# Performance work log

Measured on AMD Instinct MI355X. Metric: run time of the kernel, lower is better.

The kernel has to match this reference:

```python
import jax, jax.numpy as jnp
import numpy as np

D_MODEL = 384
N_HEADS = 8
HEAD_DIM = D_MODEL // N_HEADS


def setup_inputs() -> dict:
    key = jax.random.key(0)
    ks = jax.random.split(key, 8)
    b, n = 2, 2048
    s = 0.02
    return {
        "x": jax.random.normal(ks[0], (b, n, D_MODEL), jnp.float32),
        "coords": jax.random.normal(ks[1], (b, n, 3), jnp.float32),
        "W_qkv": jax.random.normal(ks[2], (D_MODEL, 3 * D_MODEL), jnp.float32) * s,
        "b_qkv": jnp.zeros((3 * D_MODEL,), jnp.float32),
        "W_dist": jax.random.normal(ks[3], (1, N_HEADS), jnp.float32) * s,
        "b_dist": jnp.zeros((N_HEADS,), jnp.float32),
        "W_out": jax.random.normal(ks[4], (D_MODEL, D_MODEL), jnp.float32) * s,
        "b_out": jnp.zeros((D_MODEL,), jnp.float32),
    }


def reference(x, coords, W_qkv, b_qkv, W_dist, b_dist, W_out, b_out):
    b, n, _ = x.shape
    qkv = x @ W_qkv + b_qkv                       # (b, n, 3*d)
    q, k, v = jnp.split(qkv, 3, axis=-1)
    def heads(t):
        return t.reshape(b, n, N_HEADS, HEAD_DIM).transpose(0, 2, 1, 3)  # b h n d
    q, k, v = heads(q), heads(k), heads(v)
    attn = jnp.einsum('bhid,bhjd->bhij', q, k) / jnp.sqrt(jnp.float32(HEAD_DIM))
    # distance bias: ||c_i - c_j|| projected to heads (Linear(1, n_heads))
    diff = coords[:, :, None, :] - coords[:, None, :, :]   # (b, i, j, 3)
    dist = jnp.sqrt(jnp.sum(diff * diff, axis=-1))         # (b, i, j)
    dist_bias = dist[..., None] * W_dist[0] + b_dist       # (b, i, j, h)
    attn = attn + dist_bias.transpose(0, 3, 1, 2)          # (b, h, i, j)
    attn = jax.nn.softmax(attn, axis=-1)
    out = jnp.einsum('bhij,bhjd->bhid', attn, v)
    out = out.transpose(0, 2, 1, 3).reshape(b, n, D_MODEL)
    return out @ W_out + b_out
```

## Files before the change

kernel.cpp:

```cpp
#include <hip/hip_runtime.h>
#include <hip/hip_bf16.h>

#define NB 2
#define SEQ 2048
#define DM 384
#define NH 8
#define HD 48
#define QKVN 1152
#define BH (NB*NH)

typedef __hip_bfloat16 bf16;
typedef __attribute__((ext_vector_type(8))) short short8;
typedef __attribute__((ext_vector_type(4))) float float4v;

static __device__ __forceinline__ float bf2f(bf16 v){ return __bfloat162float(v); }
static __device__ __forceinline__ float ldin(const void* p, size_t i, int isf){
    return isf ? ((const float*)p)[i] : bf2f(((const bf16*)p)[i]);
}
static __device__ __forceinline__ short f2b(float f){
    union { float f; unsigned u; } a; a.f = f;
    unsigned r = a.u + 0x7FFFu + ((a.u >> 16) & 1u);
    return (short)(r >> 16);
}
static __device__ __forceinline__ unsigned pk2(float a, float b){
    union { float f; unsigned u; } ua, ub; ua.f = a; ub.f = b;
    return ((ua.u + 0x8000u) >> 16) | ((ub.u + 0x8000u) & 0xFFFF0000u);
}
static __device__ __forceinline__ float bflo(unsigned u){
    union { unsigned u; float f; } a; a.u = u << 16; return a.f;
}
static __device__ __forceinline__ float bfhi(unsigned u){
    union { unsigned u; float f; } a; a.u = u & 0xFFFF0000u; return a.f;
}
static __device__ __forceinline__ int detect_isf(const void* x){
    const unsigned short* xb = (const unsigned short*)x;
    int l = threadIdx.x & 63;
    union { unsigned u; float f; } a; a.u = ((unsigned)xb[2*l]) << 16;
    float ab = fabsf(a.f);
    int good = (a.f == 0.0f) || (ab > 9.765625e-4f && ab < 1024.0f);
    unsigned long long m = __ballot(good);
    return (__popcll(m) >= 32) ? 0 : 1;
}

__global__ __launch_bounds__(256) void k_prep(const void* __restrict__ x,
    const void* __restrict__ coords,
    const void* __restrict__ Wqkv, const void* __restrict__ Wout,
    const void* __restrict__ bqkv, const void* __restrict__ bout,
    const void* __restrict__ Wdist, const void* __restrict__ bdist,
    short* __restrict__ dist8, short* __restrict__ xb,
    short* __restrict__ WqT, short* __restrict__ WoT,
    float* __restrict__ bqf, float* __restrict__ bof,
    float* __restrict__ wdf, float* __restrict__ bdf)
{
    const int isf = detect_isf(x);
    const int t = threadIdx.x;
    const int b = blockIdx.x;
    if (b < 512) {
        const int bb = b >> 8;
        const int j0 = (b & 255) * 8;
        __shared__ float cjx[8], cjy[8], cjz[8];
        if (t < 8) {
            int gj = (bb*SEQ + j0 + t)*3;
            cjx[t] = ldin(coords, gj, isf);
            cjy[t] = ldin(coords, gj+1, isf);
            cjz[t] = ldin(coords, gj+2, isf);
        }
        __syncthreads();
        #pragma unroll
        for (int ii = 0; ii < 8; ++ii) {
            int i = ii*256 + t;
            int gi = (bb*SEQ + i)*3;
            float px = ldin(coords, gi, isf), py = ldin(coords, gi+1, isf), pz = ldin(coords, gi+2, isf);
            short o[8];
            #pragma unroll
            for (int e = 0; e < 8; ++e) {
                float dx = px - cjx[e], dy = py - cjy[e], dz = pz - cjz[e];
                o[e] = f2b(sqrtf(dx*dx + dy*dy + dz*dz));
            }
            *(int4*)(dist8 + ((size_t)b*SEQ + i)*8) = *(const int4*)o;
        }
    } else if (b < 1280) {
        size_t i = ((size_t)(b-512)*256 + t)*8;
        if (isf) {
            const float* xf = (const float*)x + i;
            short o[8];
            #pragma unroll
            for (int e = 0; e < 8; ++e) o[e] = f2b(xf[e]);
            *(int4*)(xb + i) = *(const int4*)o;
        } else {
            *(int4*)(xb + i) = *(const int4*)((const short*)x + i);
        }
    } else if (b < 1856) {
        int bb, NW; const void* W; short* WT;
        if (b < 1712) { bb = b - 1280; NW = QKVN; W = Wqkv; WT = WqT; }
        else          { bb = b - 1712; NW = DM;   W = Wout; WT = WoT; }
        int ntiles = NW >> 5;
        int kt = bb / ntiles, nt = bb % ntiles;
        int k0 = kt*32, n0 = nt*32;
        __shared__ float Ls[32][33];
        for (int idx = t; idx < 1024; idx += 256) {
            int r = idx >> 5, c = idx & 31;
            Ls[r][c] = ldin(W, (size_t)(k0+r)*NW + n0 + c, isf);
        }
        __syncthreads();
        for (int idx = t; idx < 1024; idx += 256) {
            int r2 = idx >> 5, c2 = idx & 31;
            WT[(size_t)(n0+r2)*DM + k0 + c2] = f2b(Ls[c2][r2]);
        }
    } else {
        int idx = (b - 1856)*256 + t;
        if (idx < QKVN) bqf[idx] = ldin(bqkv, idx, isf);
        else if (idx < QKVN + DM) bof[idx - QKVN] = ldin(bout, idx - QKVN, isf);
        else if (idx < QKVN + DM + NH) wdf[idx - QKVN - DM] = ldin(Wdist, idx - QKVN - DM, isf);
        else if (idx < QKVN + DM + 2*NH) bdf[idx - QKVN - DM - NH] = ldin(bdist, idx - QKVN - DM - NH, isf);
    }
}

__global__ __launch_bounds__(256) void k_qkv(const short* __restrict__ xb,
    const short* __restrict__ WT, const float* __restrict__ bias,
    short* __restrict__ qg2, short* __restrict__ kg2, short* __restrict__ vg2)
{
    __shared__ __align__(16) short As[64*72];
    __shared__ __align__(16) short Bs[128*72];
    const int t = threadIdx.x;
    const int w = t >> 6, lane = t & 63, L = lane & 15, quad = lane >> 4;
    const int mt = blockIdx.x / 9, nt = blockIdx.x % 9;
    const int row0 = mt*64, col0 = nt*128;
    const int wm = w & 1, wn = w >> 1;
    float4v acc[2][4] = {};
    for (int k0 = 0; k0 < DM; k0 += 64) {
        __syncthreads();
        for (int c = t; c < 512; c += 256) {
            int row = c >> 3, k8 = c & 7;
            *(int4*)(&As[row*72 + k8*8]) = *(const int4*)(xb + (size_t)(row0+row)*DM + k0 + k8*8);
        }
        for (int c = t; c < 1024; c += 256) {
            int row = c >> 3, k8 = c & 7;
            *(int4*)(&Bs[row*72 + k8*8]) = *(const int4*)(WT + (size_t)(col0+row)*DM + k0 + k8*8);
        }
        __syncthreads();
        #pragma unroll
        for (int kc = 0; kc < 2; ++kc) {
            short8 a0 = *(const short8*)(&As[(32*wm + L)*72 + kc*32 + quad*8]);
            short8 a1 = *(const short8*)(&As[(32*wm + 16 + L)*72 + kc*32 + quad*8]);
            #pragma unroll
            for (int ni = 0; ni < 4; ++ni) {
                short8 bf = *(const short8*)(&Bs[(64*wn + 16*ni + L)*72 + kc*32 + quad*8]);
                acc[0][ni] = __builtin_amdgcn_mfma_f32_16x16x32_bf16(a0, bf, acc[0][ni], 0, 0, 0);
                acc[1][ni] = __builtin_amdgcn_mfma_f32_16x16x32_bf16(a1, bf, acc[1][ni], 0, 0, 0);
            }
        }
    }
    const int which = col0 / DM;
    const int cbase = col0 % DM;
    short* Ep = Bs;
    __syncthreads();
    if (which < 2) {
        #pragma unroll
        for (int mi = 0; mi < 2; ++mi)
            #pragma unroll
            for (int ni = 0; ni < 4; ++ni) {
                int col_l = 64*wn + 16*ni + L;
                float bv = bias[col0 + col_l];
                #pragma unroll
                for (int r = 0; r < 4; ++r) {
                    int row_l = 32*wm + 16*mi + quad*4 + r;
                    Ep[row_l*136 + col_l] = f2b(acc[mi][ni][r] + bv);
                }
            }
        __syncthreads();
        short* dst = which ? kg2 : qg2;
        for (int c = t; c < 1024; c += 256) {
            int row_l = c >> 4, col_l = (c & 15)*8;
            int4 val = *(const int4*)(&Ep[row_l*136 + col_l]);
            int row_g = row0 + row_l;
            int bi = row_g >> 11, nn = row_g & (SEQ-1);
            int c2 = cbase + col_l;
            int hh = c2/HD, dd = c2%HD;
            int bh = bi*NH + hh;
            size_t u = ((((size_t)bh*128 + (nn>>4))*2 + (dd>>5))*4 + ((dd>>3)&3))*128
                       + (size_t)(nn & 15)*8;
            *(int4*)(dst + u) = val;
        }
    } else {
        #pragma unroll
        for (int mi = 0; mi < 2; ++mi)
            #pragma unroll
            for (int ni = 0; ni < 4; ++ni) {
                int col_l = 64*wn + 16*ni + L;
                float bv = bias[col0 + col_l];
                #pragma unroll
                for (int r = 0; r < 4; ++r) {
                    int row_l = 32*wm + 16*mi + quad*4 + r;
                    Ep[col_l*72 + row_l] = f2b(acc[mi][ni][r] + bv);
                }
            }
        __syncthreads();
        for (int c = t; c < 1024; c += 256) {
            int col_l = c >> 3, row_l = (c & 7)*8;
            int4 val = *(const int4*)(&Ep[col_l*72 + row_l]);
            int row_g = row0 + row_l;
            int bi = row_g >> 11, nn = row_g & (SEQ-1);
            int c2 = cbase + col_l;
            int hh = c2/HD, dd = c2%HD;
            int bh = bi*NH + hh;
            size_t u = (((((size_t)bh*32 + (nn>>6))*3 + (dd>>4))*2 + ((nn>>5)&1))*4 + ((nn>>3)&3))*128
                       + (size_t)(dd & 15)*8;
            *(int4*)(vg2 + u) = val;
        }
    }
}

__global__ __launch_bounds__(256) void k_attn(
    const short* __restrict__ qg2, const short* __restrict__ kg2, const short* __restrict__ vg2,
    const short* __restrict__ dist8, const float* __restrict__ wdf,
    const float* __restrict__ bdf, float* __restrict__ partO, float* __restrict__ partL)
{
    __shared__ __align__(16) short PsT[4][16*72];
    const int t = threadIdx.x;
    const int w = t >> 6, lane = t & 63, L = lane & 15, q = lane >> 4;
    const int bid = blockIdx.x;
    const int jsb = bid & 1, it = (bid >> 1) & 31, bh = bid >> 6;
    const int bi = bh >> 3, hh = bh & 7;
    const int i0 = it*64;
    const float scale = 0.14433756729740643f;
    const float wd = wdf[hh], bd = bdf[hh];

    const short* qbase = qg2 + (((size_t)bh*128 + it*4 + w)*2)*512;
    const short8 qa0 = *(const short8*)(qbase + (q*16 + L)*8);
    const short8 qa1 = *(const short8*)(qbase + 512 + (q*16 + L)*8);

    const int iL = i0 + 16*w + L;
    float rsum = 0.f;
    float4v accO[3] = {};

    const short* kB = kg2 + (size_t)bh*131072 + (q*16 + L)*8;
    const short* vB = vg2 + (size_t)bh*98304  + (q*16 + L)*8;
    const short* dB = dist8 + (size_t)bi*256*SEQ*8 + (size_t)iL*8 + 4*(q&1);

    const int jlo = jsb*(SEQ/2), jhi = jlo + SEQ/2;

    short8 pk[2][8];
    uint2  pd[2][4];
    #pragma unroll
    for (int nt = 0; nt < 4; ++nt) {
        const short* kb = kB + (size_t)((jlo>>4) + nt)*1024;
        pk[0][nt*2]   = *(const short8*)(kb);
        pk[0][nt*2+1] = *(const short8*)(kb + 512);
        pd[0][nt] = *(const uint2*)(dB + (size_t)((jlo>>3) + 2*nt + (q>>1))*(SEQ*8));
    }

    #pragma unroll 2
    for (int j0 = jlo; j0 < jhi; j0 += 64) {
        const int p = (j0 >> 6) & 1;
        const int jn = (j0 + 64 < jhi) ? j0 + 64 : jlo;
        #pragma unroll
        for (int nt = 0; nt < 4; ++nt) {
            const short* kb = kB + (size_t)((jn>>4) + nt)*1024;
            pk[p^1][nt*2]   = *(const short8*)(kb);
            pk[p^1][nt*2+1] = *(const short8*)(kb + 512);
            pd[p^1][nt] = *(const uint2*)(dB + (size_t)((jn>>3) + 2*nt + (q>>1))*(SEQ*8));
        }
        short8 vf[6];
        #pragma unroll
        for (int dt = 0; dt < 3; ++dt) {
            const short* vb = vB + (size_t)((j0>>6)*3 + dt)*1024;
            vf[dt*2]   = *(const short8*)(vb);
            vf[dt*2+1] = *(const short8*)(vb + 512);
        }
        float4v sacc[4] = {};
        #pragma unroll
        for (int nt = 0; nt < 4; ++nt) {
            sacc[nt] = __builtin_amdgcn_mfma_f32_16x16x32_bf16(pk[p][nt*2],   qa0, sacc[nt], 0, 0, 0);
            sacc[nt] = __builtin_amdgcn_mfma_f32_16x16x32_bf16(pk[p][nt*2+1], qa1, sacc[nt], 0, 0, 0);
        }
        #pragma unroll
        for (int nt = 0; nt < 4; ++nt) {
            uint2 du = pd[p][nt];
            float d0 = bflo(du.x), d1 = bfhi(du.x), d2 = bflo(du.y), d3 = bfhi(du.y);
            float p0 = __expf(fmaf(sacc[nt][0], scale, fmaf(d0, wd, bd)));
            float p1 = __expf(fmaf(sacc[nt][1], scale, fmaf(d1, wd, bd)));
            float p2 = __expf(fmaf(sacc[nt][2], scale, fmaf(d2, wd, bd)));
            float p3 = __expf(fmaf(sacc[nt][3], scale, fmaf(d3, wd, bd)));
            rsum += (p0 + p1) + (p2 + p3);
            uint2 pw; pw.x = pk2(p0, p1); pw.y = pk2(p2, p3);
            *(uint2*)(&PsT[w][L*72 + 16*nt + 4*q]) = pw;
        }
        short8 pa0 = *(const short8*)(&PsT[w][L*72 + q*8]);
        short8 pa1 = *(const short8*)(&PsT[w][L*72 + 32 + q*8]);
        #pragma unroll
        for (int dt = 0; dt < 3; ++dt) {
            accO[dt] = __builtin_amdgcn_mfma_f32_16x16x32_bf16(pa0, vf[dt*2],   accO[dt], 0, 0, 0);
            accO[dt] = __builtin_amdgcn_mfma_f32_16x16x32_bf16(pa1, vf[dt*2+1], accO[dt], 0, 0, 0);
        }
    }
    rsum += __shfl_xor(rsum, 16);
    rsum += __shfl_xor(rsum, 32);
    const size_t pbase = ((size_t)(jsb*BH + bh))*SEQ;
    if (q == 0) partL[pbase + iL] = rsum;
    #pragma unroll
    for (int dt = 0; dt < 3; ++dt)
        #pragma unroll
        for (int r = 0; r < 4; ++r)
            partO[(pbase + i0 + 16*w + 4*q + r)*48 + 16*dt + L] = accO[dt][r];
}

__global__ __launch_bounds__(256) void k_red(const float* __restrict__ partO,
    const float* __restrict__ partL, short* __restrict__ aob)
{
    int g = blockIdx.x*256 + threadIdx.x;
    int row = g / 48, cg = g % 48;
    int bi = row >> 11, i = row & (SEQ-1);
    int hh = cg / 6, d8 = (cg % 6)*8;
    int bh = bi*NH + hh;
    size_t o0 = ((size_t)bh*SEQ + i)*48 + d8;
    size_t o1 = ((size_t)(BH + bh)*SEQ + i)*48 + d8;
    float4 a0 = *(const float4*)(partO + o0);
    float4 a1 = *(const float4*)(partO + o0 + 4);
    float4 b0 = *(const float4*)(partO + o1);
    float4 b1 = *(const float4*)(partO + o1 + 4);
    float l = partL[(size_t)bh*SEQ + i] + partL[(size_t)(BH + bh)*SEQ + i];
    float inv = 1.0f / l;
    short o[8];
    o[0] = f2b((a0.x + b0.x)*inv); o[1] = f2b((a0.y + b0.y)*inv);
    o[2] = f2b((a0.z + b0.z)*inv); o[3] = f2b((a0.w + b0.w)*inv);
    o[4] = f2b((a1.x + b1.x)*inv); o[5] = f2b((a1.y + b1.y)*inv);
    o[6] = f2b((a1.z + b1.z)*inv); o[7] = f2b((a1.w + b1.w)*inv);
    *(int4*)(aob + (size_t)row*DM + hh*HD + d8) = *(const int4*)o;
}

__global__ __launch_bounds__(256) void k_out(const short* __restrict__ aob,
    const short* __restrict__ WT, const float* __restrict__ bias,
    void* __restrict__ out, const void* __restrict__ x)
{
    __shared__ __align__(16) short As[64*72];
    __shared__ __align__(16) short Bs[128*72];
    const int isf = detect_isf(x);
    const int t = threadIdx.x;
    const int w = t >> 6, lane = t & 63, L = lane & 15, quad = lane >> 4;
    const int mt = blockIdx.x / 3, nt = blockIdx.x % 3;
    const int row0 = mt*64, col0 = nt*128;
    const int wm = w & 1, wn = w >> 1;
    float4v acc[2][4] = {};
    for (int k0 = 0; k0 < DM; k0 += 64) {
        __syncthreads();
        for (int c = t; c < 512; c += 256) {
            int row = c >> 3, k8 = c & 7;
            *(int4*)(&As[row*72 + k8*8]) = *(const int4*)(aob + (size_t)(row0+row)*DM + k0 + k8*8);
        }
        for (int c = t; c < 1024; c += 256) {
            int row = c >> 3, k8 = c & 7;
            *(int4*)(&Bs[row*72 + k8*8]) = *(const int4*)(WT + (size_t)(col0+row)*DM + k0 + k8*8);
        }
        __syncthreads();
        #pragma unroll
        for (int kc = 0; kc < 2; ++kc) {
            short8 a0 = *(const short8*)(&As[(32*wm + L)*72 + kc*32 + quad*8]);
            short8 a1 = *(const short8*)(&As[(32*wm + 16 + L)*72 + kc*32 + quad*8]);
            #pragma unroll
            for (int ni = 0; ni < 4; ++ni) {
                short8 bf = *(const short8*)(&Bs[(64*wn + 16*ni + L)*72 + kc*32 + quad*8]);
                acc[0][ni] = __builtin_amdgcn_mfma_f32_16x16x32_bf16(a0, bf, acc[0][ni], 0, 0, 0);
                acc[1][ni] = __builtin_amdgcn_mfma_f32_16x16x32_bf16(a1, bf, acc[1][ni], 0, 0, 0);
            }
        }
    }
    #pragma unroll
    for (int mi = 0; mi < 2; ++mi) {
        #pragma unroll
        for (int ni = 0; ni < 4; ++ni) {
            int col_g = col0 + 64*wn + 16*ni + L;
            float bv = bias[col_g];
            #pragma unroll
            for (int r = 0; r < 4; ++r) {
                int row_g = row0 + 32*wm + 16*mi + quad*4 + r;
                size_t oi = (size_t)row_g*DM + col_g;
                float val = acc[mi][ni][r] + bv;
                if (isf) ((float*)out)[oi] = val;
                else     ((bf16*)out)[oi]  = __float2bfloat16(val);
            }
        }
    }
}

extern "C" void kernel_launch(void* const* d_in, const int* in_sizes, int n_in,
                              void* d_out, int out_size, void* d_ws, size_t ws_size,
                              hipStream_t stream) {
    const void* x      = d_in[0];
    const void* coords = d_in[1];
    const void* Wqkv   = d_in[2];
    const void* bqkv   = d_in[3];
    const void* Wdist  = d_in[4];
    const void* bdist  = d_in[5];
    const void* Wout   = d_in[6];
    const void* bout   = d_in[7];

    short* qg2   = (short*)d_ws;
    short* kg2   = qg2  + (size_t)2097152;
    short* vg2   = kg2  + (size_t)2097152;
    short* dist8 = vg2  + (size_t)1572864;
    short* aob   = dist8 + (size_t)8388608;
    short* xb    = aob  + (size_t)1572864;
    short* WqT   = xb   + (size_t)1572864;
    short* WoT   = WqT  + (size_t)442368;
    float* partO = (float*)(WoT + (size_t)147456);
    float* partL = partO + (size_t)3145728;
    float* bqf   = partL + (size_t)65536;
    float* bof   = bqf + QKVN;
    float* wdf   = bof + DM;
    float* bdf   = wdf + NH;

    hipMemsetAsync(qg2, 0, (size_t)2*2097152*sizeof(short), stream);

    k_prep<<<dim3(1863), dim3(256), 0, stream>>>(x, coords, Wqkv, Wout, bqkv, bout,
                                                 Wdist, bdist, dist8, xb, WqT, WoT,
                                                 bqf, bof, wdf, bdf);
    k_qkv<<<dim3(64*9), dim3(256), 0, stream>>>(xb, WqT, bqf, qg2, kg2, vg2);
    k_attn<<<dim3(1024), dim3(256), 0, stream>>>(qg2, kg2, vg2, dist8, wdf, bdf,
                                                 partO, partL);
    k_red<<<dim3(768), dim3(256), 0, stream>>>(partO, partL, aob);
    k_out<<<dim3(64*3), dim3(256), 0, stream>>>(aob, WoT, bof, d_out, x);
}
```

Baseline: 179.3 us.

## Split attention key range four ways, drop register prefetch, store bf16 partials

The attention kernel now splits the key dimension into four chunks instead of two, doubling the grid so more blocks keep the GPU busy. The explicit double-buffered register prefetch of K and dist tiles is removed, K/V/dist are loaded inline next to their MFMAs, and launch bounds ask for four blocks per SM to raise occupancy. Partial outputs are stored as bf16 instead of fp32, which halves partial traffic, and the reduction kernel sums four splits. The cost is less software latency hiding, more reduction work and extra rounding of unnormalized partial sums.

```diff
diff --git a/kernel.cpp b/kernel.cpp
--- a/kernel.cpp
+++ b/kernel.cpp
@@ -8,6 +8,7 @@
 #define HD 48
 #define QKVN 1152
 #define BH (NB*NH)
+#define NSPLIT 4
 
 typedef __hip_bfloat16 bf16;
 typedef __attribute__((ext_vector_type(8))) short short8;
@@ -31,6 +32,9 @@
 }
 static __device__ __forceinline__ float bfhi(unsigned u){
     union { unsigned u; float f; } a; a.u = u & 0xFFFF0000u; return a.f;
+}
+static __device__ __forceinline__ float bfs(unsigned short s){
+    union { unsigned u; float f; } a; a.u = ((unsigned)s) << 16; return a.f;
 }
 static __device__ __forceinline__ int detect_isf(const void* x){
     const unsigned short* xb = (const unsigned short*)x;
@@ -211,16 +215,16 @@
     }
 }
 
-__global__ __launch_bounds__(256) void k_attn(
+__global__ __launch_bounds__(256, 4) void k_attn(
     const short* __restrict__ qg2, const short* __restrict__ kg2, const short* __restrict__ vg2,
     const short* __restrict__ dist8, const float* __restrict__ wdf,
-    const float* __restrict__ bdf, float* __restrict__ partO, float* __restrict__ partL)
+    const float* __restrict__ bdf, short* __restrict__ partO, float* __restrict__ partL)
 {
     __shared__ __align__(16) short PsT[4][16*72];
     const int t = threadIdx.x;
     const int w = t >> 6, lane = t & 63, L = lane & 15, q = lane >> 4;
     const int bid = blockIdx.x;
-    const int jsb = bid & 1, it = (bid >> 1) & 31, bh = bid >> 6;
+    const int jsb = bid & 3, it = (bid >> 2) & 31, bh = bid >> 7;
     const int bi = bh >> 3, hh = bh & 7;
     const int i0 = it*64;
     const float scale = 0.14433756729740643f;
@@ -234,49 +238,25 @@
     float rsum = 0.f;
     float4v accO[3] = {};
 
-    const short* kB = kg2 + (size_t)bh*131072 + (q*16 + L)*8;
-    const short* vB = vg2 + (size_t)bh*98304  + (q*16 + L)*8;
-    const short* dB = dist8 + (size_t)bi*256*SEQ*8 + (size_t)iL*8 + 4*(q&1);
-
-    const int jlo = jsb*(SEQ/2), jhi = jlo + SEQ/2;
-
-    short8 pk[2][8];
-    uint2  pd[2][4];
-    #pragma unroll
-    for (int nt = 0; nt < 4; ++nt) {
-        const short* kb = kB + (size_t)((jlo>>4) + nt)*1024;
-        pk[0][nt*2]   = *(const short8*)(kb);
-        pk[0][nt*2+1] = *(const short8*)(kb + 512);
-        pd[0][nt] = *(const uint2*)(dB + (size_t)((jlo>>3) + 2*nt + (q>>1))*(SEQ*8));
-    }
-
-    #pragma unroll 2
+    const size_t kBH = (size_t)bh*131072;
+    const size_t vBH = (size_t)bh*98304;
+    const size_t dB  = (size_t)bi*256*SEQ*8;
+
+    const int jlo = jsb*(SEQ/NSPLIT), jhi = jlo + SEQ/NSPLIT;
     for (int j0 = jlo; j0 < jhi; j0 += 64) {
-        const int p = (j0 >> 6) & 1;
-        const int jn = (j0 + 64 < jhi) ? j0 + 64 : jlo;
+        float4v sacc[4] = {};
         #pragma unroll
         for (int nt = 0; nt < 4; ++nt) {
-            const short* kb = kB + (size_t)((jn>>4) + nt)*1024;
-            pk[p^1][nt*2]   = *(const short8*)(kb);
-            pk[p^1][nt*2+1] = *(const short8*)(kb + 512);
-            pd[p^1][nt] = *(const uint2*)(dB + (size_t)((jn>>3) + 2*nt + (q>>1))*(SEQ*8));
-        }
-        short8 vf[6];
-        #pragma unroll
-        for (int dt = 0; dt < 3; ++dt) {
-            const short* vb = vB + (size_t)((j0>>6)*3 + dt)*1024;
-            vf[dt*2]   = *(const short8*)(vb);
-            vf[dt*2+1] = *(const short8*)(vb + 512);
-        }
-        float4v sacc[4] = {};
+            const short* kb = kg2 + kBH + ((size_t)((j0>>4) + nt))*1024;
+            short8 kf0 = *(const short8*)(kb + (q*16 + L)*8);
+            sacc[nt] = __builtin_amdgcn_mfma_f32_16x16x32_bf16(kf0, qa0, sacc[nt], 0, 0, 0);
+            short8 kf1 = *(const short8*)(kb + 512 + (q*16 + L)*8);
+            sacc[nt] = __builtin_amdgcn_mfma_f32_16x16x32_bf16(kf1, qa1, sacc[nt], 0, 0, 0);
+        }
         #pragma unroll
         for (int nt = 0; nt < 4; ++nt) {
-            sacc[nt] = __builtin_amdgcn_mfma_f32_16x16x32_bf16(pk[p][nt*2],   qa0, sacc[nt], 0, 0, 0);
-            sacc[nt] = __builtin_amdgcn_mfma_f32_16x16x32_bf16(pk[p][nt*2+1], qa1, sacc[nt], 0, 0, 0);
-        }
-        #pragma unroll
-        for (int nt = 0; nt < 4; ++nt) {
-            uint2 du = pd[p][nt];
+            const short* dp = dist8 + dB + (((size_t)(j0>>6)*8 + 2*nt + (q>>1))*SEQ + iL)*8 + 4*(q&1);
+            uint2 du = *(const uint2*)dp;
             float d0 = bflo(du.x), d1 = bfhi(du.x), d2 = bflo(du.y), d3 = bfhi(du.y);
             float p0 = __expf(fmaf(sacc[nt][0], scale, fmaf(d0, wd, bd)));
             float p1 = __expf(fmaf(sacc[nt][1], scale, fmaf(d1, wd, bd)));
@@ -290,8 +270,11 @@
         short8 pa1 = *(const short8*)(&PsT[w][L*72 + 32 + q*8]);
         #pragma unroll
         for (int dt = 0; dt < 3; ++dt) {
-            accO[dt] = __builtin_amdgcn_mfma_f32_16x16x32_bf16(pa0, vf[dt*2],   accO[dt], 0, 0, 0);
-            accO[dt] = __builtin_amdgcn_mfma_f32_16x16x32_bf16(pa1, vf[dt*2+1], accO[dt], 0, 0, 0);
+            const short* vb = vg2 + vBH + ((size_t)(j0>>6)*3 + dt)*1024;
+            short8 vf0 = *(const short8*)(vb + (q*16 + L)*8);
+            accO[dt] = __builtin_amdgcn_mfma_f32_16x16x32_bf16(pa0, vf0, accO[dt], 0, 0, 0);
+            short8 vf1 = *(const short8*)(vb + 512 + (q*16 + L)*8);
+            accO[dt] = __builtin_amdgcn_mfma_f32_16x16x32_bf16(pa1, vf1, accO[dt], 0, 0, 0);
         }
     }
     rsum += __shfl_xor(rsum, 16);
@@ -302,10 +285,10 @@
     for (int dt = 0; dt < 3; ++dt)
         #pragma unroll
         for (int r = 0; r < 4; ++r)
-            partO[(pbase + i0 + 16*w + 4*q + r)*48 + 16*dt + L] = accO[dt][r];
-}
-
-__global__ __launch_bounds__(256) void k_red(const float* __restrict__ partO,
+            partO[(pbase + i0 + 16*w + 4*q + r)*48 + 16*dt + L] = f2b(accO[dt][r]);
+}
+
+__global__ __launch_bounds__(256) void k_red(const short* __restrict__ partO,
     const float* __restrict__ partL, short* __restrict__ aob)
 {
     int g = blockIdx.x*256 + threadIdx.x;
@@ -313,19 +296,22 @@
     int bi = row >> 11, i = row & (SEQ-1);
     int hh = cg / 6, d8 = (cg % 6)*8;
     int bh = bi*NH + hh;
-    size_t o0 = ((size_t)bh*SEQ + i)*48 + d8;
-    size_t o1 = ((size_t)(BH + bh)*SEQ + i)*48 + d8;
-    float4 a0 = *(const float4*)(partO + o0);
-    float4 a1 = *(const float4*)(partO + o0 + 4);
-    float4 b0 = *(const float4*)(partO + o1);
-    float4 b1 = *(const float4*)(partO + o1 + 4);
-    float l = partL[(size_t)bh*SEQ + i] + partL[(size_t)(BH + bh)*SEQ + i];
+    float acc[8] = {};
+    float l = 0.f;
+    #pragma unroll
+    for (int s = 0; s < NSPLIT; ++s) {
+        const short* p = partO + ((size_t)(s*BH + bh)*SEQ + i)*48 + d8;
+        uint4 u = *(const uint4*)p;
+        acc[0] += bflo(u.x); acc[1] += bfhi(u.x);
+        acc[2] += bflo(u.y); acc[3] += bfhi(u.y);
+        acc[4] += bflo(u.z); acc[5] += bfhi(u.z);
+        acc[6] += bflo(u.w); acc[7] += bfhi(u.w);
+        l += partL[(size_t)(s*BH + bh)*SEQ + i];
+    }
     float inv = 1.0f / l;
     short o[8];
-    o[0] = f2b((a0.x + b0.x)*inv); o[1] = f2b((a0.y + b0.y)*inv);
-    o[2] = f2b((a0.z + b0.z)*inv); o[3] = f2b((a0.w + b0.w)*inv);
-    o[4] = f2b((a1.x + b1.x)*inv); o[5] = f2b((a1.y + b1.y)*inv);
-    o[6] = f2b((a1.z + b1.z)*inv); o[7] = f2b((a1.w + b1.w)*inv);
+    #pragma unroll
+    for (int e = 0; e < 8; ++e) o[e] = f2b(acc[e]*inv);
     *(int4*)(aob + (size_t)row*DM + hh*HD + d8) = *(const int4*)o;
 }
 
@@ -403,9 +389,9 @@
     short* xb    = aob  + (size_t)1572864;
     short* WqT   = xb   + (size_t)1572864;
     short* WoT   = WqT  + (size_t)442368;
-    float* partO = (float*)(WoT + (size_t)147456);
-    float* partL = partO + (size_t)3145728;
-    float* bqf   = partL + (size_t)65536;
+    short* partO = WoT  + (size_t)147456;
+    float* partL = (float*)(partO + (size_t)NSPLIT*BH*SEQ*48);
+    float* bqf   = partL + (size_t)NSPLIT*BH*SEQ;
     float* bof   = bqf + QKVN;
     float* wdf   = bof + DM;
     float* bdf   = wdf + NH;
@@ -416,8 +402,8 @@
                                                  Wdist, bdist, dist8, xb, WqT, WoT,
                                                  bqf, bof, wdf, bdf);
     k_qkv<<<dim3(64*9), dim3(256), 0, stream>>>(xb, WqT, bqf, qg2, kg2, vg2);
-    k_attn<<<dim3(1024), dim3(256), 0, stream>>>(qg2, kg2, vg2, dist8, wdf, bdf,
-                                                 partO, partL);
+    k_attn<<<dim3(16*32*NSPLIT), dim3(256), 0, stream>>>(qg2, kg2, vg2, dist8, wdf, bdf,
+                                                         partO, partL);
     k_red<<<dim3(768), dim3(256), 0, stream>>>(partO, partL, aob);
     k_out<<<dim3(64*3), dim3(256), 0, stream>>>(aob, WoT, bof, d_out, x);
 }
```

New measurement: 165.8 us. 1.08x faster.
